# Optimization experiments

Hardware: AMD Instinct MI355X
Metric: run time of the kernel (lower is better)

## Reference

```python
import jax, jax.numpy as jnp
import numpy as np

N_HEAD, N_MIX, D_MODEL, D_K, D_V = 8, 2, 512, 64, 64
BN_EPS = 1e-5


def avg_pool_3x3_s2(x):
    # AvgPool2d(kernel=3, stride=2, pad=1, count_include_pad=False) on NCHW
    win = (1, 1, 3, 3)
    stride = (1, 1, 2, 2)
    pad = [(0, 0), (0, 0), (1, 1), (1, 1)]
    s = jax.lax.reduce_window(x, 0.0, jax.lax.add, win, stride, pad)
    ones = jnp.ones((1, 1, x.shape[2], x.shape[3]), x.dtype)
    cnt = jax.lax.reduce_window(ones, 0.0, jax.lax.add, win, stride, pad)
    return s / cnt


def conv1x1(x, w, b=None):
    # w: [out_c, in_c]; x: [B, in_c, H, W]
    y = jnp.einsum('oc,bchw->bohw', w, x)
    if b is not None:
        y = y + b[None, :, None, None]
    return y


def setup_inputs() -> dict:
    key = jax.random.key(0)
    ks = jax.random.split(key, 8)
    B, H, W = 2, 56, 56
    std_kq = np.sqrt(2.0 / (D_MODEL + D_K)).astype(np.float32)
    std_v = np.sqrt(2.0 / (D_MODEL + D_V)).astype(np.float32)
    std_mix = np.power(N_MIX, -0.5).astype(np.float32)
    return {
        'x': jax.random.normal(ks[0], (B, D_MODEL, H, W), jnp.float32),
        'w_qs': jax.random.normal(ks[1], (N_HEAD * D_K, D_MODEL), jnp.float32) * std_kq,
        'b_qs': jnp.zeros((N_HEAD * D_K,), jnp.float32),
        'w_vs': jax.random.normal(ks[2], (N_HEAD * D_V, D_MODEL), jnp.float32) * std_v,
        'b_vs': jnp.zeros((N_HEAD * D_V,), jnp.float32),
        'mix_w': jax.random.uniform(ks[3], (N_MIX, D_K), jnp.float32, -std_mix, std_mix),
        'w_out': jax.random.normal(ks[4], (D_MODEL, N_HEAD * D_V), jnp.float32) * 0.02,
        'bn_gamma': jnp.ones((D_MODEL,), jnp.float32),
        'bn_beta': jnp.zeros((D_MODEL,), jnp.float32),
    }


def reference(x, w_qs, b_qs, w_vs, b_vs, mix_w, w_out, bn_gamma, bn_beta):
    B, C, H, W = x.shape
    N = H * W
    m = N_MIX
    d = D_K // m  # per-mixture dim
    temperature = D_K ** 0.5

    px = avg_pool_3x3_s2(x)  # [B, C, H/2, W/2]
    N2 = px.shape[2] * px.shape[3]

    # conv_ks aliases conv_qs in the original (shared weights)
    qt = conv1x1(x, w_qs, b_qs).reshape(B * N_HEAD, D_K, N)
    kt = conv1x1(px, w_qs, b_qs).reshape(B * N_HEAD, D_K, N2)
    vt = conv1x1(px, w_vs, b_vs).reshape(B * N_HEAD, D_V, N2)

    # mixture weights pi: softmax over mixtures of weight @ mean_q
    bar_qt = qt.mean(axis=2)  # [B', D_K]
    pi = jax.nn.softmax(jnp.einsum('md,bd->bm', mix_w, bar_qt), axis=1)  # [B', m]

    q = qt.reshape(B * N_HEAD * m, d, N).transpose(0, 2, 1)  # [B'm, N, d]
    k2 = kt.reshape(B * N_HEAD * m, d, N2)  # [B'm, d, N2]

    attn = jnp.einsum('bnd,bdk->bnk', q, k2) / temperature  # [B'm, N, N2]
    attn = jax.nn.softmax(attn, axis=2)
    # dropout is identity in eval mode
    attn = (attn * pi.reshape(-1, 1, 1)).reshape(B * N_HEAD, m, N, N2).sum(1)

    out = jnp.einsum('bnk,bvk->bnv', attn, vt)  # [B', N, D_V]
    out = out.transpose(0, 2, 1).reshape(B, N_HEAD * D_V, H, W)
    out = conv1x1(out, w_out)  # no bias
    # BatchNorm2d in eval mode: running_mean=0, running_var=1
    inv = 1.0 / jnp.sqrt(jnp.float32(1.0 + BN_EPS))
    out = out * inv * bn_gamma[None, :, None, None] + bn_beta[None, :, None, None]
    return out + x
```

## Files before the change

### kernel.cpp

```cpp
#include <hip/hip_runtime.h>
#include <math.h>

typedef unsigned short u16;
typedef short bf16x8 __attribute__((ext_vector_type(8)));
typedef float f32x4 __attribute__((ext_vector_type(4)));

#define MFMA(a, b, c) __builtin_amdgcn_mfma_f32_16x16x32_bf16(a, b, c, 0, 0, 0)

#define SCALE_K 0.18033688011112043f

__device__ __forceinline__ float bf2f(u16 v) {
    union { float f; unsigned u; } x;
    x.u = ((unsigned)v) << 16;
    return x.f;
}
__device__ __forceinline__ u16 f2bf(float f) {
    union { float f; unsigned u; } x;
    x.f = f;
    unsigned r = x.u + 0x7FFF + ((x.u >> 16) & 1);
    return (u16)(r >> 16);
}

__global__ __launch_bounds__(256) void cvt_kernel(const float* __restrict__ s0,
                                                  const float* __restrict__ s1,
                                                  const float* __restrict__ s2,
                                                  u16* __restrict__ d0, u16* __restrict__ d1,
                                                  u16* __restrict__ d2) {
    int i = blockIdx.x * 256 + threadIdx.x;
    const float* s = (blockIdx.y == 0) ? s0 : ((blockIdx.y == 1) ? s1 : s2);
    u16* d = (blockIdx.y == 0) ? d0 : ((blockIdx.y == 1) ? d1 : d2);
    d[i] = f2bf(s[i]);
}

__global__ __launch_bounds__(256) void transpose_kernel(const float* __restrict__ x,
                                                        u16* __restrict__ xT) {
    __shared__ u16 tile[64][65];
    int b = blockIdx.z;
    int n0 = blockIdx.x * 64, c0 = blockIdx.y * 64;
    int j = threadIdx.x & 63, q = threadIdx.x >> 6;
    const float* xb = x + b * 512 * 3136;
#pragma unroll
    for (int it = 0; it < 16; ++it) {
        int r = q * 16 + it;
        tile[r][j] = f2bf(xb[(c0 + r) * 3136 + n0 + j]);
    }
    __syncthreads();
    u16* xTb = xT + b * 3136 * 512;
#pragma unroll
    for (int it = 0; it < 16; ++it) {
        int r = q * 16 + it;
        xTb[(n0 + r) * 512 + c0 + j] = tile[j][r];
    }
}

__global__ __launch_bounds__(256) void pool_kernel(const u16* __restrict__ xT,
                                                   u16* __restrict__ pxT) {
    int n2 = blockIdx.x;
    int b = blockIdx.y;
    int t = threadIdx.x;
    int i = n2 / 28, jj = n2 % 28;
    float s0 = 0.f, s1 = 0.f;
    int cnt = 0;
    const u16* xb = xT + b * 3136 * 512;
#pragma unroll
    for (int dr = 0; dr < 3; dr++) {
        int r = 2 * i - 1 + dr;
        if (r < 0 || r >= 56) continue;
#pragma unroll
        for (int dc = 0; dc < 3; dc++) {
            int cc = 2 * jj - 1 + dc;
            if (cc < 0 || cc >= 56) continue;
            const u16* row = xb + (r * 56 + cc) * 512;
            s0 += bf2f(row[t]);
            s1 += bf2f(row[t + 256]);
            cnt++;
        }
    }
    float invc = 1.0f / (float)cnt;
    u16* op = pxT + (b * 784 + n2) * 512;
    op[t] = f2bf(s0 * invc);
    op[t + 256] = f2bf(s1 * invc);
}

__device__ __forceinline__ void gemm_core(const u16* __restrict__ A, int lda, int M,
                                          const u16* __restrict__ BT, int ldb, int Ncol,
                                          int K, int row0, int col0, f32x4 acc[4][4]) {
    int lane = threadIdx.x & 63;
    int lr = lane & 15, lg = lane >> 4;
    int ar[4], bc[4];
#pragma unroll
    for (int i = 0; i < 4; i++) {
        int r = row0 + i * 16 + lr;
        ar[i] = (r < M) ? r : (M - 1);
    }
#pragma unroll
    for (int j = 0; j < 4; j++) {
        int cj = col0 + j * 16 + lr;
        bc[j] = (cj < Ncol) ? cj : (Ncol - 1);
    }
    for (int k = 0; k < K; k += 32) {
        int ko = k + lg * 8;
        bf16x8 af[4], bfr[4];
#pragma unroll
        for (int i = 0; i < 4; i++) af[i] = *(const bf16x8*)(A + ar[i] * lda + ko);
#pragma unroll
        for (int j = 0; j < 4; j++) bfr[j] = *(const bf16x8*)(BT + bc[j] * ldb + ko);
#pragma unroll
        for (int i = 0; i < 4; i++)
#pragma unroll
            for (int j = 0; j < 4; j++) acc[i][j] = MFMA(af[i], bfr[j], acc[i][j]);
    }
}

__global__ __launch_bounds__(256) void gemm_qk(const u16* __restrict__ xT,
                                               const u16* __restrict__ W,
                                               const float* __restrict__ bias,
                                               u16* __restrict__ out, int M, int Npad,
                                               float oscale) {
    int b = blockIdx.z;
    int w = threadIdx.x >> 6;
    int row0 = blockIdx.y * 128 + (w >> 1) * 64;
    int col0 = blockIdx.x * 128 + (w & 1) * 64;
    f32x4 acc[4][4];
#pragma unroll
    for (int i = 0; i < 4; i++)
#pragma unroll
        for (int j = 0; j < 4; j++) acc[i][j] = (f32x4){0.f, 0.f, 0.f, 0.f};
    gemm_core(xT + b * M * 512, 512, M, W, 512, 512, 512, row0, col0, acc);
    int lane = threadIdx.x & 63;
    int lr = lane & 15, lg = lane >> 4;
#pragma unroll
    for (int j = 0; j < 4; j++) {
        int oc = col0 + j * 16 + lr;
        float bs = bias[oc];
        int bh = b * 8 + (oc >> 6), dk = oc & 63;
        u16* op = out + (bh * Npad) * 64 + dk;
#pragma unroll
        for (int i = 0; i < 4; i++) {
#pragma unroll
            for (int r = 0; r < 4; r++) {
                int n = row0 + i * 16 + lg * 4 + r;
                if (n < M) op[n * 64] = f2bf((acc[i][j][r] + bs) * oscale);
                else if (n < Npad) op[n * 64] = 0;
            }
        }
    }
}

__global__ __launch_bounds__(256) void gemm_v(const u16* __restrict__ W,
                                              const u16* __restrict__ pxT,
                                              const float* __restrict__ bias,
                                              u16* __restrict__ vt) {
    int b = blockIdx.z;
    int w = threadIdx.x >> 6;
    int row0 = blockIdx.y * 128 + (w >> 1) * 64;
    int col0 = blockIdx.x * 128 + (w & 1) * 64;
    f32x4 acc[4][4];
#pragma unroll
    for (int i = 0; i < 4; i++)
#pragma unroll
        for (int j = 0; j < 4; j++) acc[i][j] = (f32x4){0.f, 0.f, 0.f, 0.f};
    gemm_core(W, 512, 512, pxT + b * 784 * 512, 512, 784, 512, row0, col0, acc);
    int lane = threadIdx.x & 63;
    int lr = lane & 15, lg = lane >> 4;
#pragma unroll
    for (int i = 0; i < 4; i++) {
#pragma unroll
        for (int r = 0; r < 4; r++) {
            int oc = row0 + i * 16 + lg * 4 + r;
            float bs = bias[oc];
            u16* vp = vt + ((b * 8 + (oc >> 6)) * 80 + (oc & 63)) * 800;
#pragma unroll
            for (int j = 0; j < 4; j++) {
                int n2 = col0 + j * 16 + lr;
                if (n2 < 784) vp[n2] = f2bf(acc[i][j][r] + bs);
                else if (n2 < 800) vp[n2] = 0;
            }
        }
    }
}

__global__ __launch_bounds__(256) void vpad_kernel(u16* __restrict__ vt) {
    int idx = blockIdx.x * 256 + threadIdx.x;
    int col = idx % 800;
    int row = (idx / 800) & 15;
    int bh = idx / (16 * 800);
    u16 v = (row == 0 && col < 784) ? (u16)0x3F80 : (u16)0;
    vt[(bh * 80 + 64 + row) * 800 + col] = v;
}

__global__ __launch_bounds__(256) void pi_stage1(const u16* __restrict__ qt,
                                                 float* __restrict__ part) {
    __shared__ float red[4][64];
    int chunk = blockIdx.x, bh = blockIdx.y;
    int t = threadIdx.x, dk = t & 63, seg = t >> 6;
    const u16* q = qt + (bh * 3136 + chunk * 112) * 64 + dk;
    float s = 0.f;
    for (int n = seg; n < 112; n += 4) s += bf2f(q[n * 64]);
    red[seg][dk] = s;
    __syncthreads();
    if (t < 64) part[(bh * 28 + chunk) * 64 + t] =
        red[0][t] + red[1][t] + red[2][t] + red[3][t];
}

__global__ __launch_bounds__(64) void pi_stage2(const float* __restrict__ part,
                                                const float* __restrict__ mix_w,
                                                float* __restrict__ pi) {
    int bh = blockIdx.x, lane = threadIdx.x;
    float bar = 0.f;
#pragma unroll
    for (int c = 0; c < 28; c++) bar += part[(bh * 28 + c) * 64 + lane];
    bar *= (1.0f / 3136.0f);
    float l0 = mix_w[lane] * bar;
    float l1 = mix_w[64 + lane] * bar;
#pragma unroll
    for (int d = 1; d < 64; d <<= 1) {
        l0 += __shfl_xor(l0, d);
        l1 += __shfl_xor(l1, d);
    }
    if (lane == 0) {
        float mx = fmaxf(l0, l1);
        float e0 = __expf(l0 - mx), e1 = __expf(l1 - mx);
        float inv = 1.0f / (e0 + e1);
        pi[bh * 2 + 0] = e0 * inv;
        pi[bh * 2 + 1] = e1 * inv;
    }
}

__global__ __launch_bounds__(256) void attn_kernel(const u16* __restrict__ qt,
                                                   const u16* __restrict__ kt,
                                                   const u16* __restrict__ vt,
                                                   const float* __restrict__ pi,
                                                   u16* __restrict__ ao) {
    __shared__ __attribute__((aligned(16))) u16 p_lds[4][2][16][40];
    int w = threadIdx.x >> 6, lane = threadIdx.x & 63;
    int lr = lane & 15, lg = lane >> 4;
    int bh = blockIdx.x & 15;
    int xq = blockIdx.x >> 4;
    int qbase = (xq * 4 + w) * 16;
    const u16* qp = qt + (bh * 3136 + qbase) * 64;
    const u16* kp = kt + bh * 800 * 64;
    const u16* vp = vt + bh * 80 * 800;

    bf16x8 qf[2];
    qf[0] = *(const bf16x8*)(qp + lr * 64 + lg * 8);
    qf[1] = *(const bf16x8*)(qp + lr * 64 + 32 + lg * 8);

    f32x4 O[2][4], Osum[2];
#pragma unroll
    for (int m = 0; m < 2; m++) {
#pragma unroll
        for (int t = 0; t < 4; t++) O[m][t] = (f32x4){0.f, 0.f, 0.f, 0.f};
        Osum[m] = (f32x4){0.f, 0.f, 0.f, 0.f};
    }

    auto loadV = [&](int base, bf16x8* vf, bf16x8& vfs) {
#pragma unroll
        for (int t = 0; t < 4; t++)
            vf[t] = *(const bf16x8*)(vp + (t * 16 + lr) * 800 + base + lg * 8);
        vfs = *(const bf16x8*)(vp + (64 + lr) * 800 + base + lg * 8);
    };
    auto loadK = [&](int base, bf16x8 (*kf)[2]) {
#pragma unroll
        for (int m = 0; m < 2; m++) {
            kf[m][0] = *(const bf16x8*)(kp + (base + lr) * 64 + m * 32 + lg * 8);
            kf[m][1] = *(const bf16x8*)(kp + (base + 16 + lr) * 64 + m * 32 + lg * 8);
        }
    };
    auto compute = [&](bf16x8* vf, bf16x8& vfs, bf16x8 (*kf)[2]) {
#pragma unroll
        for (int m = 0; m < 2; m++) {
            f32x4 s0 = MFMA(qf[m], kf[m][0], ((f32x4){0.f, 0.f, 0.f, 0.f}));
            f32x4 s1 = MFMA(qf[m], kf[m][1], ((f32x4){0.f, 0.f, 0.f, 0.f}));
#pragma unroll
            for (int r = 0; r < 4; r++) {
                float p0 = __builtin_amdgcn_exp2f(s0[r]);
                float p1 = __builtin_amdgcn_exp2f(s1[r]);
                unsigned u;
                asm("v_cvt_pk_bf16_f32 %0, %1, %2" : "=v"(u) : "v"(p0), "v"(p1));
                p_lds[w][m][lg * 4 + r][lr] = (u16)u;
                p_lds[w][m][lg * 4 + r][16 + lr] = (u16)(u >> 16);
            }
        }
#pragma unroll
        for (int m = 0; m < 2; m++) {
            bf16x8 pf = *(const bf16x8*)(&p_lds[w][m][lr][lg * 8]);
#pragma unroll
            for (int t = 0; t < 4; t++) O[m][t] = MFMA(pf, vf[t], O[m][t]);
            Osum[m] = MFMA(pf, vfs, Osum[m]);
        }
    };

    bf16x8 vfA[4], vfsA, kfA[2][2];
    bf16x8 vfB[4], vfsB, kfB[2][2];
    loadV(0, vfA, vfsA);
    loadK(0, kfA);
    for (int c = 0; c < 24; c += 2) {
        loadV((c + 1) * 32, vfB, vfsB);
        loadK((c + 1) * 32, kfB);
        compute(vfA, vfsA, kfA);
        loadV((c + 2) * 32, vfA, vfsA);
        loadK((c + 2) * 32, kfA);
        compute(vfB, vfsB, kfB);
    }
    compute(vfA, vfsA, kfA);

    float pi0 = pi[bh * 2], pi1 = pi[bh * 2 + 1];
    float inv0[4], inv1[4];
#pragma unroll
    for (int r = 0; r < 4; r++) {
        float l0 = __shfl(Osum[0][r], lane & 48);
        float l1 = __shfl(Osum[1][r], lane & 48);
        inv0[r] = pi0 / l0;
        inv1[r] = pi1 / l1;
    }
    int b = bh >> 3, h = bh & 7;
    u16* aop = ao + ((b * 3136 + qbase) * 512) + h * 64;
#pragma unroll
    for (int t = 0; t < 4; t++) {
#pragma unroll
        for (int r = 0; r < 4; r++) {
            int n = lg * 4 + r;
            float v = inv0[r] * O[0][t][r] + inv1[r] * O[1][t][r];
            aop[n * 512 + t * 16 + lr] = f2bf(v);
        }
    }
}

__global__ __launch_bounds__(256) void gemm_out(const u16* __restrict__ W,
                                                const u16* __restrict__ aoT,
                                                const float* __restrict__ gamma,
                                                const float* __restrict__ beta,
                                                const float* __restrict__ xres,
                                                float* __restrict__ out) {
    int b = blockIdx.z;
    int w = threadIdx.x >> 6;
    int row0 = blockIdx.y * 128 + (w >> 1) * 64;
    int col0 = blockIdx.x * 128 + (w & 1) * 64;
    f32x4 acc[4][4];
#pragma unroll
    for (int i = 0; i < 4; i++)
#pragma unroll
        for (int j = 0; j < 4; j++) acc[i][j] = (f32x4){0.f, 0.f, 0.f, 0.f};
    gemm_core(W, 512, 512, aoT + b * 3136 * 512, 512, 3136, 512, row0, col0, acc);
    const float inv = 0.99999500003749969f;
    int lane = threadIdx.x & 63;
    int lr = lane & 15, lg = lane >> 4;
#pragma unroll
    for (int i = 0; i < 4; i++) {
#pragma unroll
        for (int r = 0; r < 4; r++) {
            int oc = row0 + i * 16 + lg * 4 + r;
            float g = gamma[oc] * inv;
            float bt = beta[oc];
            const float* xp = xres + (b * 512 + oc) * 3136;
            float* op = out + (b * 512 + oc) * 3136;
#pragma unroll
            for (int j = 0; j < 4; j++) {
                int n = col0 + j * 16 + lr;
                if (n < 3136) op[n] = acc[i][j][r] * g + bt + xp[n];
            }
        }
    }
}

extern "C" void kernel_launch(void* const* d_in, const int* in_sizes, int n_in,
                              void* d_out, int out_size, void* d_ws, size_t ws_size,
                              hipStream_t stream) {
    const float* x = (const float*)d_in[0];
    const float* w_qs = (const float*)d_in[1];
    const float* b_qs = (const float*)d_in[2];
    const float* w_vs = (const float*)d_in[3];
    const float* b_vs = (const float*)d_in[4];
    const float* mix_w = (const float*)d_in[5];
    const float* w_out = (const float*)d_in[6];
    const float* gamma = (const float*)d_in[7];
    const float* beta = (const float*)d_in[8];
    float* out = (float*)d_out;

    char* ws = (char*)d_ws;
    u16* xT = (u16*)(ws + 0);
    u16* ao = (u16*)(ws + 0);
    u16* pxT = (u16*)(ws + 6422528);
    u16* qt = (u16*)(ws + 8028160);
    u16* kt = (u16*)(ws + 14450688);
    u16* vt = (u16*)(ws + 16089088);
    u16* wq_b = (u16*)(ws + 18137088);
    u16* wv_b = (u16*)(ws + 18661376);
    u16* wo_b = (u16*)(ws + 19185664);
    float* pi = (float*)(ws + 19709952);
    float* part = (float*)(ws + 19710080);

    hipLaunchKernelGGL(cvt_kernel, dim3(1024, 3), dim3(256), 0, stream, w_qs, w_vs, w_out,
                       wq_b, wv_b, wo_b);
    hipLaunchKernelGGL(transpose_kernel, dim3(49, 8, 2), dim3(256), 0, stream, x, xT);
    hipLaunchKernelGGL(pool_kernel, dim3(784, 2), dim3(256), 0, stream, xT, pxT);
    hipLaunchKernelGGL(gemm_qk, dim3(4, 25, 2), dim3(256), 0, stream, xT, wq_b, b_qs, qt,
                       3136, 3136, 1.0f);
    hipLaunchKernelGGL(gemm_qk, dim3(4, 7, 2), dim3(256), 0, stream, pxT, wq_b, b_qs, kt,
                       784, 800, SCALE_K);
    hipLaunchKernelGGL(gemm_v, dim3(7, 4, 2), dim3(256), 0, stream, wv_b, pxT, b_vs, vt);
    hipLaunchKernelGGL(vpad_kernel, dim3(800), dim3(256), 0, stream, vt);
    hipLaunchKernelGGL(pi_stage1, dim3(28, 16), dim3(256), 0, stream, qt, part);
    hipLaunchKernelGGL(pi_stage2, dim3(16), dim3(64), 0, stream, part, mix_w, pi);
    hipLaunchKernelGGL(attn_kernel, dim3(784), dim3(256), 0, stream, qt, kt, vt, pi, ao);
    hipLaunchKernelGGL(gemm_out, dim3(25, 4, 2), dim3(256), 0, stream, wo_b, ao, gamma,
                       beta, x, out);
}
```

Before: 228.9 us.

## Keep attention probabilities in registers via transposed S MFMA and drop the ones-row sum

The QK^T MFMA is computed with operands swapped, so each lane's exp results already match the A-operand layout of the PV MFMA. This removes the LDS round trip for P and the per-wave shared buffer. The softmax denominator is now summed in registers with shuffles instead of an extra MFMA against a padded ones row. That removes the V padding rows, the vpad kernel and one MFMA per tile. V is now loaded as two 4-element halves per tile, and the tail tile masks its out-of-range half explicitly.

```diff
diff --git a/kernel.cpp b/kernel.cpp
--- a/kernel.cpp
+++ b/kernel.cpp
@@ -3,6 +3,7 @@
 
 typedef unsigned short u16;
 typedef short bf16x8 __attribute__((ext_vector_type(8)));
+typedef short bf16x4 __attribute__((ext_vector_type(4)));
 typedef float f32x4 __attribute__((ext_vector_type(4)));
 
 #define MFMA(a, b, c) __builtin_amdgcn_mfma_f32_16x16x32_bf16(a, b, c, 0, 0, 0)
@@ -19,6 +20,12 @@
     x.f = f;
     unsigned r = x.u + 0x7FFF + ((x.u >> 16) & 1);
     return (u16)(r >> 16);
+}
+__device__ __forceinline__ bf16x4 pk4(float a, float b, float c, float d) {
+    union { unsigned u[2]; bf16x4 v; } x;
+    asm("v_cvt_pk_bf16_f32 %0, %1, %2" : "=v"(x.u[0]) : "v"(a), "v"(b));
+    asm("v_cvt_pk_bf16_f32 %0, %1, %2" : "=v"(x.u[1]) : "v"(c), "v"(d));
+    return x.v;
 }
 
 __global__ __launch_bounds__(256) void cvt_kernel(const float* __restrict__ s0,
@@ -169,7 +176,7 @@
         for (int r = 0; r < 4; r++) {
             int oc = row0 + i * 16 + lg * 4 + r;
             float bs = bias[oc];
-            u16* vp = vt + ((b * 8 + (oc >> 6)) * 80 + (oc & 63)) * 800;
+            u16* vp = vt + ((b * 8 + (oc >> 6)) * 64 + (oc & 63)) * 800;
 #pragma unroll
             for (int j = 0; j < 4; j++) {
                 int n2 = col0 + j * 16 + lr;
@@ -178,15 +185,6 @@
             }
         }
     }
-}
-
-__global__ __launch_bounds__(256) void vpad_kernel(u16* __restrict__ vt) {
-    int idx = blockIdx.x * 256 + threadIdx.x;
-    int col = idx % 800;
-    int row = (idx / 800) & 15;
-    int bh = idx / (16 * 800);
-    u16 v = (row == 0 && col < 784) ? (u16)0x3F80 : (u16)0;
-    vt[(bh * 80 + 64 + row) * 800 + col] = v;
 }
 
 __global__ __launch_bounds__(256) void pi_stage1(const u16* __restrict__ qt,
@@ -232,7 +230,6 @@
                                                    const u16* __restrict__ vt,
                                                    const float* __restrict__ pi,
                                                    u16* __restrict__ ao) {
-    __shared__ __attribute__((aligned(16))) u16 p_lds[4][2][16][40];
     int w = threadIdx.x >> 6, lane = threadIdx.x & 63;
     int lr = lane & 15, lg = lane >> 4;
     int bh = blockIdx.x & 15;
@@ -240,26 +237,19 @@
     int qbase = (xq * 4 + w) * 16;
     const u16* qp = qt + (bh * 3136 + qbase) * 64;
     const u16* kp = kt + bh * 800 * 64;
-    const u16* vp = vt + bh * 80 * 800;
+    const u16* vp = vt + bh * 64 * 800;
 
     bf16x8 qf[2];
     qf[0] = *(const bf16x8*)(qp + lr * 64 + lg * 8);
     qf[1] = *(const bf16x8*)(qp + lr * 64 + 32 + lg * 8);
 
-    f32x4 O[2][4], Osum[2];
-#pragma unroll
-    for (int m = 0; m < 2; m++) {
+    f32x4 O[2][4];
+    float lsum[2] = {0.f, 0.f};
+#pragma unroll
+    for (int m = 0; m < 2; m++)
 #pragma unroll
         for (int t = 0; t < 4; t++) O[m][t] = (f32x4){0.f, 0.f, 0.f, 0.f};
-        Osum[m] = (f32x4){0.f, 0.f, 0.f, 0.f};
-    }
-
-    auto loadV = [&](int base, bf16x8* vf, bf16x8& vfs) {
-#pragma unroll
-        for (int t = 0; t < 4; t++)
-            vf[t] = *(const bf16x8*)(vp + (t * 16 + lr) * 800 + base + lg * 8);
-        vfs = *(const bf16x8*)(vp + (64 + lr) * 800 + base + lg * 8);
-    };
+
     auto loadK = [&](int base, bf16x8 (*kf)[2]) {
 #pragma unroll
         for (int m = 0; m < 2; m++) {
@@ -267,53 +257,61 @@
             kf[m][1] = *(const bf16x8*)(kp + (base + 16 + lr) * 64 + m * 32 + lg * 8);
         }
     };
-    auto compute = [&](bf16x8* vf, bf16x8& vfs, bf16x8 (*kf)[2]) {
+    auto loadV = [&](int base, bf16x4* v0, bf16x4* v1) {
+#pragma unroll
+        for (int t = 0; t < 4; t++) {
+            v0[t] = *(const bf16x4*)(vp + (t * 16 + lr) * 800 + base + lg * 4);
+            v1[t] = *(const bf16x4*)(vp + (t * 16 + lr) * 800 + base + 16 + lg * 4);
+        }
+    };
+    auto compute = [&](bf16x8 (*kf)[2], bf16x4* v0, bf16x4* v1, bool tail) {
 #pragma unroll
         for (int m = 0; m < 2; m++) {
-            f32x4 s0 = MFMA(qf[m], kf[m][0], ((f32x4){0.f, 0.f, 0.f, 0.f}));
-            f32x4 s1 = MFMA(qf[m], kf[m][1], ((f32x4){0.f, 0.f, 0.f, 0.f}));
-#pragma unroll
-            for (int r = 0; r < 4; r++) {
-                float p0 = __builtin_amdgcn_exp2f(s0[r]);
-                float p1 = __builtin_amdgcn_exp2f(s1[r]);
-                unsigned u;
-                asm("v_cvt_pk_bf16_f32 %0, %1, %2" : "=v"(u) : "v"(p0), "v"(p1));
-                p_lds[w][m][lg * 4 + r][lr] = (u16)u;
-                p_lds[w][m][lg * 4 + r][16 + lr] = (u16)(u >> 16);
+            f32x4 s0 = MFMA(kf[m][0], qf[m], ((f32x4){0.f, 0.f, 0.f, 0.f}));
+            f32x4 s1 = MFMA(kf[m][1], qf[m], ((f32x4){0.f, 0.f, 0.f, 0.f}));
+            float p0 = __builtin_amdgcn_exp2f(s0[0]);
+            float p1 = __builtin_amdgcn_exp2f(s0[1]);
+            float p2 = __builtin_amdgcn_exp2f(s0[2]);
+            float p3 = __builtin_amdgcn_exp2f(s0[3]);
+            float p4 = __builtin_amdgcn_exp2f(s1[0]);
+            float p5 = __builtin_amdgcn_exp2f(s1[1]);
+            float p6 = __builtin_amdgcn_exp2f(s1[2]);
+            float p7 = __builtin_amdgcn_exp2f(s1[3]);
+            if (tail) { p4 = 0.f; p5 = 0.f; p6 = 0.f; p7 = 0.f; }
+            lsum[m] += ((p0 + p1) + (p2 + p3)) + ((p4 + p5) + (p6 + p7));
+            union { bf16x4 h[2]; bf16x8 w8; } pa;
+            pa.h[0] = pk4(p0, p1, p2, p3);
+            pa.h[1] = pk4(p4, p5, p6, p7);
+#pragma unroll
+            for (int t = 0; t < 4; t++) {
+                union { bf16x4 h[2]; bf16x8 w8; } vv;
+                vv.h[0] = v0[t];
+                vv.h[1] = v1[t];
+                O[m][t] = MFMA(pa.w8, vv.w8, O[m][t]);
             }
         }
-#pragma unroll
-        for (int m = 0; m < 2; m++) {
-            bf16x8 pf = *(const bf16x8*)(&p_lds[w][m][lr][lg * 8]);
-#pragma unroll
-            for (int t = 0; t < 4; t++) O[m][t] = MFMA(pf, vf[t], O[m][t]);
-            Osum[m] = MFMA(pf, vfs, Osum[m]);
-        }
     };
 
-    bf16x8 vfA[4], vfsA, kfA[2][2];
-    bf16x8 vfB[4], vfsB, kfB[2][2];
-    loadV(0, vfA, vfsA);
+    bf16x8 kfA[2][2], kfB[2][2];
+    bf16x4 v0A[4], v1A[4], v0B[4], v1B[4];
     loadK(0, kfA);
+    loadV(0, v0A, v1A);
     for (int c = 0; c < 24; c += 2) {
-        loadV((c + 1) * 32, vfB, vfsB);
         loadK((c + 1) * 32, kfB);
-        compute(vfA, vfsA, kfA);
-        loadV((c + 2) * 32, vfA, vfsA);
+        loadV((c + 1) * 32, v0B, v1B);
+        compute(kfA, v0A, v1A, false);
         loadK((c + 2) * 32, kfA);
-        compute(vfB, vfsB, kfB);
-    }
-    compute(vfA, vfsA, kfA);
-
+        loadV((c + 2) * 32, v0A, v1A);
+        compute(kfB, v0B, v1B, false);
+    }
+    compute(kfA, v0A, v1A, true);
+
+#pragma unroll
+    for (int m = 0; m < 2; m++) {
+        lsum[m] += __shfl_xor(lsum[m], 16);
+        lsum[m] += __shfl_xor(lsum[m], 32);
+    }
     float pi0 = pi[bh * 2], pi1 = pi[bh * 2 + 1];
-    float inv0[4], inv1[4];
-#pragma unroll
-    for (int r = 0; r < 4; r++) {
-        float l0 = __shfl(Osum[0][r], lane & 48);
-        float l1 = __shfl(Osum[1][r], lane & 48);
-        inv0[r] = pi0 / l0;
-        inv1[r] = pi1 / l1;
-    }
     int b = bh >> 3, h = bh & 7;
     u16* aop = ao + ((b * 3136 + qbase) * 512) + h * 64;
 #pragma unroll
@@ -321,7 +319,9 @@
 #pragma unroll
         for (int r = 0; r < 4; r++) {
             int n = lg * 4 + r;
-            float v = inv0[r] * O[0][t][r] + inv1[r] * O[1][t][r];
+            float l0 = __shfl(lsum[0], n);
+            float l1 = __shfl(lsum[1], n);
+            float v = (pi0 / l0) * O[0][t][r] + (pi1 / l1) * O[1][t][r];
             aop[n * 512 + t * 16 + lr] = f2bf(v);
         }
     }
@@ -385,11 +385,11 @@
     u16* qt = (u16*)(ws + 8028160);
     u16* kt = (u16*)(ws + 14450688);
     u16* vt = (u16*)(ws + 16089088);
-    u16* wq_b = (u16*)(ws + 18137088);
-    u16* wv_b = (u16*)(ws + 18661376);
-    u16* wo_b = (u16*)(ws + 19185664);
-    float* pi = (float*)(ws + 19709952);
-    float* part = (float*)(ws + 19710080);
+    u16* wq_b = (u16*)(ws + 17727488);
+    u16* wv_b = (u16*)(ws + 18251776);
+    u16* wo_b = (u16*)(ws + 18776064);
+    float* pi = (float*)(ws + 19300352);
+    float* part = (float*)(ws + 19300480);
 
     hipLaunchKernelGGL(cvt_kernel, dim3(1024, 3), dim3(256), 0, stream, w_qs, w_vs, w_out,
                        wq_b, wv_b, wo_b);
@@ -400,7 +400,6 @@
     hipLaunchKernelGGL(gemm_qk, dim3(4, 7, 2), dim3(256), 0, stream, pxT, wq_b, b_qs, kt,
                        784, 800, SCALE_K);
     hipLaunchKernelGGL(gemm_v, dim3(7, 4, 2), dim3(256), 0, stream, wv_b, pxT, b_vs, vt);
-    hipLaunchKernelGGL(vpad_kernel, dim3(800), dim3(256), 0, stream, vt);
     hipLaunchKernelGGL(pi_stage1, dim3(28, 16), dim3(256), 0, stream, qt, part);
     hipLaunchKernelGGL(pi_stage2, dim3(16), dim3(64), 0, stream, part, mix_w, pi);
     hipLaunchKernelGGL(attn_kernel, dim3(784), dim3(256), 0, stream, qt, kt, vt, pi, ao);
```

Result: slower. 242.7 us (+6.0%).
